# Kernel optimization log

Hardware: AMD Instinct MI355X
Metric: run time of the kernel (lower is better)

## Reference

```python
import jax, jax.numpy as jnp
import numpy as np

B, S = 8, 2048
CHANNELS, DIM, HEADS = 256, 3, 6
TCH = CHANNELS * 2  # 512
EPS = 1e-5


def _linear_init(key, out_f, in_f):
    # torch nn.Linear default init: U(-1/sqrt(in_f), 1/sqrt(in_f)) for W and b
    k1, k2 = jax.random.split(key)
    bound = 1.0 / np.sqrt(in_f)
    w = jax.random.uniform(k1, (out_f, in_f), jnp.float32, -bound, bound)
    b = jax.random.uniform(k2, (out_f,), jnp.float32, -bound, bound)
    return w, b


def setup_inputs() -> dict:
    key = jax.random.key(0)
    ks = jax.random.split(key, 8)
    x = jax.random.normal(ks[0], (B, S, TCH), jnp.float32)
    wq, bq = _linear_init(ks[1], DIM, TCH)
    wk, bk = _linear_init(ks[2], DIM, TCH)
    wv, bv = _linear_init(ks[3], DIM, TCH)
    wo, bo = _linear_init(ks[4], TCH, HEADS * DIM)
    w1, b1 = _linear_init(ks[5], TCH, TCH)
    w2, b2 = _linear_init(ks[6], TCH, TCH)
    gamma = jnp.ones((TCH,), jnp.float32)
    beta = jnp.zeros((TCH,), jnp.float32)
    return {"x": x, "wq": wq, "bq": bq, "wk": wk, "bk": bk, "wv": wv, "bv": bv,
            "wo": wo, "bo": bo, "w1": w1, "b1": b1, "w2": w2, "b2": b2,
            "gamma": gamma, "beta": beta}


def _layernorm(x, gamma, beta):
    mu = jnp.mean(x, axis=-1, keepdims=True)
    var = jnp.mean(jnp.square(x - mu), axis=-1, keepdims=True)
    return (x - mu) * jax.lax.rsqrt(var + EPS) * gamma + beta


def reference(x, wq, bq, wk, bk, wv, bv, wo, bo, w1, b1, w2, b2, gamma, beta):
    # All heads share the same w_q/w_k/w_v, so one attention pass suffices;
    # concatenating HEADS copies reproduces the original math exactly.
    q = x @ wq.T + bq                      # [B,S,DIM]
    k = x @ wk.T + bk                      # [B,S,DIM]
    v = x @ wv.T + bv                      # [B,S,DIM]
    scores = jnp.einsum('bqd,bkd->bqk', q, k) / np.sqrt(DIM)  # [B,S,S]
    soft = jax.nn.softmax(scores, axis=-1)
    z = jnp.einsum('bqk,bkd->bqd', soft, v)  # [B,S,DIM]
    z = jnp.concatenate([z] * HEADS, axis=-1)  # [B,S,HEADS*DIM]
    z = z @ wo.T + bo                       # [B,S,TCH]
    r0 = x + (z @ w1.T + b1)
    r1 = _layernorm(r0, gamma, beta)
    r1 = r1 @ w2.T + b2
    r = r0 + r1
    return _layernorm(r, gamma, beta)
```

## Files before the change

### kernel.cpp

```cpp
#include <hip/hip_runtime.h>
#include <hip/hip_bf16.h>

#define TCH 512
#define MTOT 16384
#define SEQ 2048
#define LN_EPS 1e-5f

typedef __attribute__((ext_vector_type(8))) __bf16 bf16x8;
typedef __attribute__((ext_vector_type(4))) float f32x4;

__device__ __forceinline__ unsigned pkbf(float a, float b) {
  union { __hip_bfloat16 h; unsigned short u; } ca, cb;
  ca.h = __float2bfloat16(a); cb.h = __float2bfloat16(b);
  return (unsigned)ca.u | ((unsigned)cb.u << 16);
}
__device__ __forceinline__ float bf_lo(unsigned u) { return __uint_as_float(u << 16); }
__device__ __forceinline__ float bf_hi(unsigned u) { return __uint_as_float(u & 0xffff0000u); }

__device__ __forceinline__ bf16x8 cvt8(float4 a, float4 b) {
  union { __hip_bfloat16 h; __bf16 v; } u;
  bf16x8 r;
  u.h = __float2bfloat16(a.x); r[0] = u.v;
  u.h = __float2bfloat16(a.y); r[1] = u.v;
  u.h = __float2bfloat16(a.z); r[2] = u.v;
  u.h = __float2bfloat16(a.w); r[3] = u.v;
  u.h = __float2bfloat16(b.x); r[4] = u.v;
  u.h = __float2bfloat16(b.y); r[5] = u.v;
  u.h = __float2bfloat16(b.z); r[6] = u.v;
  u.h = __float2bfloat16(b.w); r[7] = u.v;
  return r;
}

#define QSCALE 0.8329517853860118f

__global__ __launch_bounds__(256) void prep_kernel(
    const float* __restrict__ w2,
    const float* __restrict__ wo, const float* __restrict__ bo,
    const float* __restrict__ wq, const float* __restrict__ bq,
    const float* __restrict__ wk, const float* __restrict__ bk,
    const float* __restrict__ wv, const float* __restrict__ bv,
    __hip_bfloat16* __restrict__ w2b,
    float4* __restrict__ wo_eff4,
    __hip_bfloat16* __restrict__ wqkvb, float* __restrict__ qkvbias)
{
  int i = blockIdx.x * 256 + threadIdx.x;
  w2b[i] = __float2bfloat16(w2[i]);
  if (i < TCH) {
    float s0 = 0.f, s1 = 0.f, s2 = 0.f;
    #pragma unroll
    for (int h = 0; h < 6; ++h) {
      s0 += wo[i*18 + h*3 + 0];
      s1 += wo[i*18 + h*3 + 1];
      s2 += wo[i*18 + h*3 + 2];
    }
    wo_eff4[i] = make_float4(s0, s1, s2, bo[i]);
  }
  if (i < 16 * TCH) {
    int row = i >> 9, k = i & 511;
    float v;
    if      (row < 3) v = wq[row * TCH + k] * QSCALE;
    else if (row < 6) v = wk[(row - 3) * TCH + k];
    else if (row < 9) v = wv[(row - 6) * TCH + k];
    else              v = 0.f;
    wqkvb[i] = __float2bfloat16(v);
  }
  if (i < 16) {
    float v;
    if      (i < 3) v = bq[i] * QSCALE;
    else if (i < 6) v = bk[i - 3];
    else if (i < 9) v = bv[i - 6];
    else            v = 0.f;
    qkvbias[i] = v;
  }
}

__global__ __launch_bounds__(256) void prep2_kernel(
    const float* __restrict__ w1, const float* __restrict__ b1,
    const float4* __restrict__ wo_eff4, float4* __restrict__ weff4)
{
  const int t = threadIdx.x, w = t >> 6, l = t & 63;
  const int i = blockIdx.x * 4 + w;
  float sx = 0.f, sy = 0.f, sz = 0.f, sw = 0.f;
  #pragma unroll
  for (int j = 0; j < 8; ++j) {
    const int k = j * 64 + l;
    const float a = w1[(size_t)i * TCH + k];
    const float4 e = wo_eff4[k];
    sx += a * e.x; sy += a * e.y; sz += a * e.z; sw += a * e.w;
  }
  #pragma unroll
  for (int off = 1; off < 64; off <<= 1) {
    sx += __shfl_xor(sx, off, 64);
    sy += __shfl_xor(sy, off, 64);
    sz += __shfl_xor(sz, off, 64);
    sw += __shfl_xor(sw, off, 64);
  }
  if (l == 0) weff4[i] = make_float4(sx, sy, sz, sw + b1[i]);
}

__global__ __launch_bounds__(256) void qkv_kernel(
    const float* __restrict__ x,
    const __hip_bfloat16* __restrict__ wqkvb, const float* __restrict__ qkvbias,
    float4* __restrict__ q4, uint4* __restrict__ kvp)
{
  const int t = threadIdx.x, wv = t >> 6, ln = t & 63;
  const int l16 = ln & 15, quad = ln >> 4;
  const int row0 = blockIdx.x * 16;
  const int k0 = wv * 128;

  bf16x8 bfr[4];
  #pragma unroll
  for (int ks = 0; ks < 4; ++ks)
    bfr[ks] = *reinterpret_cast<const bf16x8*>(wqkvb + l16 * TCH + k0 + ks * 32 + quad * 8);

  const float* xp = x + (size_t)(row0 + l16) * TCH + k0 + quad * 8;

  f32x4 acc = {};
  #pragma unroll
  for (int ks = 0; ks < 4; ++ks) {
    float4 a = *(const float4*)(xp + ks * 32);
    float4 b = *(const float4*)(xp + ks * 32 + 4);
    acc = __builtin_amdgcn_mfma_f32_16x16x32_bf16(cvt8(a, b), bfr[ks], acc, 0, 0, 0);
  }

  __shared__ float tr[4][16][17];
  __shared__ float fin[16][17];
  #pragma unroll
  for (int r = 0; r < 4; ++r) tr[wv][quad * 4 + r][l16] = acc[r];
  __syncthreads();

  {
    const int r = t >> 4, c = t & 15;
    fin[r][c] = tr[0][r][c] + tr[1][r][c] + tr[2][r][c] + tr[3][r][c] + qkvbias[c];
  }
  __syncthreads();

  if (t < 16) {
    q4[row0 + t] = make_float4(fin[t][0], fin[t][1], fin[t][2], 0.f);
  } else if (t < 32) {
    const int r = t - 16;
    kvp[row0 + r] = make_uint4(pkbf(fin[r][3], fin[r][4]),
                               pkbf(fin[r][5], fin[r][6]),
                               pkbf(fin[r][7], fin[r][8]), 0u);
  }
}

__global__ __launch_bounds__(1024) void attn_kernel(
    const float4* __restrict__ q4, const uint4* __restrict__ kvp,
    const float* __restrict__ x, const float4* __restrict__ weff4,
    const float* __restrict__ gamma, const float* __restrict__ beta,
    __hip_bfloat16* __restrict__ r0b, __hip_bfloat16* __restrict__ r1b)
{
  __shared__ float4 part[16 * 64];
  __shared__ float4 zbuf[64];

  const int b    = blockIdx.x >> 5;
  const int qc   = blockIdx.x & 31;
  const int base = b * SEQ;
  const int tid  = threadIdx.x;
  const int wave = tid >> 6;
  const int lane = tid & 63;
  const float4 q = q4[base + qc * 64 + lane];

  const int wu = __builtin_amdgcn_readfirstlane(wave);
  const uint4* kvw = kvp + base + wu * 128;

  float l[4] = {}, a0[4] = {}, a1[4] = {}, a2[4] = {};
  #pragma unroll 4
  for (int i = 0; i < 32; ++i) {
    #pragma unroll
    for (int s = 0; s < 4; ++s) {
      uint4 rec = kvw[s * 32 + i];
      float sc = bf_lo(rec.x) * q.x + bf_hi(rec.x) * q.y + bf_lo(rec.y) * q.z;
      float p = __builtin_amdgcn_exp2f(sc);
      l[s]  += p;
      a0[s] += p * bf_hi(rec.y);
      a1[s] += p * bf_lo(rec.z);
      a2[s] += p * bf_hi(rec.z);
    }
  }
  part[wave * 64 + lane] = make_float4(l[0]+l[1]+l[2]+l[3],
                                       a0[0]+a0[1]+a0[2]+a0[3],
                                       a1[0]+a1[1]+a1[2]+a1[3],
                                       a2[0]+a2[1]+a2[2]+a2[3]);
  __syncthreads();

  if (tid < 64) {
    float L = 0.f, A0 = 0.f, A1 = 0.f, A2 = 0.f;
    #pragma unroll
    for (int w = 0; w < 16; ++w) {
      float4 p = part[w * 64 + tid];
      L += p.x; A0 += p.y; A1 += p.z; A2 += p.w;
    }
    const float inv = 1.f / L;
    zbuf[tid] = make_float4(A0 * inv, A1 * inv, A2 * inv, 0.f);
  }
  __syncthreads();

  const int c0 = lane * 8;
  float4 wv[8];
  #pragma unroll
  for (int j = 0; j < 8; ++j) wv[j] = weff4[c0 + j];
  const float4 g0  = *(const float4*)(gamma + c0);
  const float4 g1  = *(const float4*)(gamma + c0 + 4);
  const float4 be0 = *(const float4*)(beta  + c0);
  const float4 be1 = *(const float4*)(beta  + c0 + 4);
  const float gg[8] = {g0.x,g0.y,g0.z,g0.w,g1.x,g1.y,g1.z,g1.w};
  const float bb[8] = {be0.x,be0.y,be0.z,be0.w,be1.x,be1.y,be1.z,be1.w};

  #pragma unroll
  for (int qi = 0; qi < 4; ++qi) {
    const int qloc = wave * 4 + qi;
    const int grow = base + qc * 64 + qloc;
    const float4 z = zbuf[qloc];
    const float* xr = x + (size_t)grow * TCH + c0;
    const float4 x0 = *(const float4*)xr;
    const float4 x1 = *(const float4*)(xr + 4);
    const float xv[8] = {x0.x,x0.y,x0.z,x0.w,x1.x,x1.y,x1.z,x1.w};
    float r0v[8], s = 0.f, sq = 0.f;
    #pragma unroll
    for (int j = 0; j < 8; ++j) {
      float v = xv[j] + z.x * wv[j].x + z.y * wv[j].y + z.z * wv[j].z + wv[j].w;
      r0v[j] = v; s += v; sq += v * v;
    }
    #pragma unroll
    for (int off = 1; off < 64; off <<= 1) {
      s  += __shfl_xor(s,  off, 64);
      sq += __shfl_xor(sq, off, 64);
    }
    const float mu = s * (1.f / TCH);
    const float rs = rsqrtf(sq * (1.f / TCH) - mu * mu + LN_EPS);
    *(bf16x8*)(r0b + (size_t)grow * TCH + c0) =
        cvt8(make_float4(r0v[0], r0v[1], r0v[2], r0v[3]),
             make_float4(r0v[4], r0v[5], r0v[6], r0v[7]));
    float r1v[8];
    #pragma unroll
    for (int j = 0; j < 8; ++j) r1v[j] = (r0v[j] - mu) * rs * gg[j] + bb[j];
    *(bf16x8*)(r1b + (size_t)grow * TCH + c0) =
        cvt8(make_float4(r1v[0], r1v[1], r1v[2], r1v[3]),
             make_float4(r1v[4], r1v[5], r1v[6], r1v[7]));
  }
}

__global__ __launch_bounds__(512) void gemm2_kernel(
    const __hip_bfloat16* __restrict__ A,
    const __hip_bfloat16* __restrict__ W,
    const float* __restrict__ bias,
    const __hip_bfloat16* __restrict__ res,
    const float* __restrict__ gamma, const float* __restrict__ beta,
    float* __restrict__ out)
{
  __shared__ __align__(16) __hip_bfloat16 At[2][4][32][8];
  __shared__ __align__(16) __hip_bfloat16 Wt[2][4][512][8];
  __shared__ float redS[32][4], redQ[32][4];
  __shared__ float muL[32], rsL[32];

  const int row0 = blockIdx.x * 32;
  const int t    = threadIdx.x;
  const int w    = t >> 6;
  const int l    = t & 63;
  const int l16  = l & 15, quad = l >> 4;
  const int wr   = w >> 2, wc = w & 3;

  auto stage = [&](int ks, int buf) {
    if (t < 128) {
      const int srow = t & 31, qa = t >> 5;
      __builtin_amdgcn_global_load_lds(
          (const __attribute__((address_space(1))) void*)(A + (size_t)(row0 + srow) * TCH + ks * 32 + qa * 8),
          (__attribute__((address_space(3))) void*)&At[buf][qa][srow][0], 16, 0, 0);
    }
    #pragma unroll
    for (int j = 0; j < 4; ++j) {
      __builtin_amdgcn_global_load_lds(
          (const __attribute__((address_space(1))) void*)(W + (size_t)t * TCH + ks * 32 + j * 8),
          (__attribute__((address_space(3))) void*)&Wt[buf][j][t][0], 16, 0, 0);
    }
  };

  f32x4 acc[8] = {};
  stage(0, 0);
  for (int ks = 0; ks < 16; ++ks) {
    const int cur = ks & 1;
    __syncthreads();
    if (ks < 15) stage(ks + 1, cur ^ 1);
    bf16x8 af, bfv[8];
    af = *reinterpret_cast<const bf16x8*>(&At[cur][quad][wr * 16 + l16][0]);
    #pragma unroll
    for (int n = 0; n < 8; ++n)
      bfv[n] = *reinterpret_cast<const bf16x8*>(&Wt[cur][quad][wc * 128 + n * 16 + l16][0]);
    #pragma unroll
    for (int n = 0; n < 8; ++n)
      acc[n] = __builtin_amdgcn_mfma_f32_16x16x32_bf16(af, bfv[n], acc[n], 0, 0, 0);
  }

  #pragma unroll
  for (int r = 0; r < 4; ++r) {
    const int lrow = wr * 16 + quad * 4 + r;
    const int grow = row0 + lrow;
    float s = 0.f, sq = 0.f;
    #pragma unroll
    for (int n = 0; n < 8; ++n) {
      const int col = wc * 128 + n * 16 + l16;
      float v = acc[n][r] + bias[col] +
                __bfloat162float(res[(size_t)grow * TCH + col]);
      acc[n][r] = v; s += v; sq += v * v;
    }
    #pragma unroll
    for (int off = 1; off < 16; off <<= 1) {
      s  += __shfl_xor(s,  off, 64);
      sq += __shfl_xor(sq, off, 64);
    }
    if (l16 == 0) { redS[lrow][wc] = s; redQ[lrow][wc] = sq; }
  }
  __syncthreads();
  if (t < 32) {
    const float S = redS[t][0] + redS[t][1] + redS[t][2] + redS[t][3];
    const float Q = redQ[t][0] + redQ[t][1] + redQ[t][2] + redQ[t][3];
    const float mu = S * (1.f / TCH);
    muL[t] = mu;
    rsL[t] = rsqrtf(Q * (1.f / TCH) - mu * mu + LN_EPS);
  }
  __syncthreads();
  #pragma unroll
  for (int r = 0; r < 4; ++r) {
    const int lrow = wr * 16 + quad * 4 + r;
    const int grow = row0 + lrow;
    const float mu = muL[lrow], rs = rsL[lrow];
    #pragma unroll
    for (int n = 0; n < 8; ++n) {
      const int col = wc * 128 + n * 16 + l16;
      out[(size_t)grow * TCH + col] =
          (acc[n][r] - mu) * rs * gamma[col] + beta[col];
    }
  }
}

extern "C" void kernel_launch(void* const* d_in, const int* in_sizes, int n_in,
                              void* d_out, int out_size, void* d_ws, size_t ws_size,
                              hipStream_t stream) {
  (void)in_sizes; (void)n_in; (void)out_size; (void)ws_size;
  const float* x     = (const float*)d_in[0];
  const float* wq    = (const float*)d_in[1];
  const float* bq    = (const float*)d_in[2];
  const float* wk    = (const float*)d_in[3];
  const float* bk    = (const float*)d_in[4];
  const float* wv    = (const float*)d_in[5];
  const float* bv    = (const float*)d_in[6];
  const float* wo    = (const float*)d_in[7];
  const float* bo    = (const float*)d_in[8];
  const float* w1    = (const float*)d_in[9];
  const float* b1    = (const float*)d_in[10];
  const float* w2    = (const float*)d_in[11];
  const float* b2    = (const float*)d_in[12];
  const float* gamma = (const float*)d_in[13];
  const float* beta  = (const float*)d_in[14];
  float* out = (float*)d_out;

  char* ws = (char*)d_ws;
  size_t off = 0;
  float4* q4      = (float4*)(ws + off); off += (size_t)MTOT * 16;
  uint4*  kvp     = (uint4*)(ws + off);  off += (size_t)MTOT * 16;
  float4* wo_eff4 = (float4*)(ws + off); off += (size_t)TCH * 16;
  float4* weff4   = (float4*)(ws + off); off += (size_t)TCH * 16;
  __hip_bfloat16* w2b   = (__hip_bfloat16*)(ws + off); off += (size_t)TCH * TCH * 2;
  __hip_bfloat16* wqkvb = (__hip_bfloat16*)(ws + off); off += (size_t)16 * TCH * 2;
  float*          qkvbias = (float*)(ws + off);        off += 64;
  __hip_bfloat16* r0b = (__hip_bfloat16*)(ws + off); off += (size_t)MTOT * TCH * 2;
  __hip_bfloat16* r1b = (__hip_bfloat16*)(ws + off); off += (size_t)MTOT * TCH * 2;

  prep_kernel<<<(TCH*TCH)/256, 256, 0, stream>>>(
      w2, wo, bo, wq, bq, wk, bk, wv, bv, w2b, wo_eff4, wqkvb, qkvbias);
  prep2_kernel<<<TCH/4, 256, 0, stream>>>(w1, b1, wo_eff4, weff4);
  qkv_kernel<<<MTOT/16, 256, 0, stream>>>(x, wqkvb, qkvbias, q4, kvp);
  attn_kernel<<<MTOT/64, 1024, 0, stream>>>(q4, kvp, x, weff4, gamma, beta, r0b, r1b);
  gemm2_kernel<<<MTOT/32, 512, 0, stream>>>(r1b, w2b, b2, r0b, gamma, beta, out);
}
```

Measured before the change: 195.8 us.

## Load gemm2 operands directly from global memory instead of LDS staging

Removes the double-buffered LDS staging (global_load_lds plus per-step __syncthreads) in gemm2 and has each lane read its MFMA A and W fragments straight from global memory, fully unrolling the K loop. The goal is to eliminate barrier stalls and LDS traffic and to let the compiler hoist and overlap loads. The cost is that the W tile is now fetched separately by each of the two wave rows rather than shared through LDS, which relies on L1/L2 caching. The reads are also 16-byte accesses strided by a full row, so they may coalesce less well.

```diff
diff --git a/kernel.cpp b/kernel.cpp
--- a/kernel.cpp
+++ b/kernel.cpp
@@ -250,8 +250,6 @@
     const float* __restrict__ gamma, const float* __restrict__ beta,
     float* __restrict__ out)
 {
-  __shared__ __align__(16) __hip_bfloat16 At[2][4][32][8];
-  __shared__ __align__(16) __hip_bfloat16 Wt[2][4][512][8];
   __shared__ float redS[32][4], redQ[32][4];
   __shared__ float muL[32], rsL[32];
 
@@ -262,35 +260,18 @@
   const int l16  = l & 15, quad = l >> 4;
   const int wr   = w >> 2, wc = w & 3;
 
-  auto stage = [&](int ks, int buf) {
-    if (t < 128) {
-      const int srow = t & 31, qa = t >> 5;
-      __builtin_amdgcn_global_load_lds(
-          (const __attribute__((address_space(1))) void*)(A + (size_t)(row0 + srow) * TCH + ks * 32 + qa * 8),
-          (__attribute__((address_space(3))) void*)&At[buf][qa][srow][0], 16, 0, 0);
-    }
-    #pragma unroll
-    for (int j = 0; j < 4; ++j) {
-      __builtin_amdgcn_global_load_lds(
-          (const __attribute__((address_space(1))) void*)(W + (size_t)t * TCH + ks * 32 + j * 8),
-          (__attribute__((address_space(3))) void*)&Wt[buf][j][t][0], 16, 0, 0);
-    }
-  };
+  const __hip_bfloat16* Ap = A + (size_t)(row0 + wr * 16 + l16) * TCH + quad * 8;
+  const __hip_bfloat16* Wp = W + (size_t)(wc * 128 + l16) * TCH + quad * 8;
 
   f32x4 acc[8] = {};
-  stage(0, 0);
+  #pragma unroll
   for (int ks = 0; ks < 16; ++ks) {
-    const int cur = ks & 1;
-    __syncthreads();
-    if (ks < 15) stage(ks + 1, cur ^ 1);
-    bf16x8 af, bfv[8];
-    af = *reinterpret_cast<const bf16x8*>(&At[cur][quad][wr * 16 + l16][0]);
-    #pragma unroll
-    for (int n = 0; n < 8; ++n)
-      bfv[n] = *reinterpret_cast<const bf16x8*>(&Wt[cur][quad][wc * 128 + n * 16 + l16][0]);
-    #pragma unroll
-    for (int n = 0; n < 8; ++n)
-      acc[n] = __builtin_amdgcn_mfma_f32_16x16x32_bf16(af, bfv[n], acc[n], 0, 0, 0);
+    bf16x8 af = *reinterpret_cast<const bf16x8*>(Ap + ks * 32);
+    #pragma unroll
+    for (int n = 0; n < 8; ++n) {
+      bf16x8 bfv = *reinterpret_cast<const bf16x8*>(Wp + (size_t)n * 16 * TCH + ks * 32);
+      acc[n] = __builtin_amdgcn_mfma_f32_16x16x32_bf16(af, bfv, acc[n], 0, 0, 0);
+    }
   }
 
   #pragma unroll
```

New measurement: 209.5 us. +7.0%, slower.
